# Performance work log

Measured on AMD Instinct MI355X. Metric: run time of the kernel, lower is better.

Reference implementation:

```python
import jax, jax.numpy as jnp
import numpy as np
import math

B, U, IN, H = 4096, 6, 256, 600
IKS, IVS, NIH = 64, 400, 1           # input attention key/value sizes, heads
CKS, CQS, NCH = 32, 32, 4            # comm attention key/query sizes, heads
CVS = H                              # comm value size forced to hidden_size
K = 4                                # top-k active units


@jax.custom_vjp
def blocked_grad(x, mask):
    return x

def _bg_fwd(x, mask):
    return x, mask

def _bg_bwd(mask, g):
    return (g * mask, jnp.zeros_like(mask))

blocked_grad.defvjp(_bg_fwd, _bg_bwd)


def _gll(x, w):
    # GroupLinearLayer: per-unit bmm, x (B,U,din) @ w (U,din,dout) -> (B,U,dout)
    return jnp.einsum('bud,udo->buo', x, w)


def setup_inputs() -> dict:
    key = jax.random.key(0)
    ks = jax.random.split(key, 16)
    r = lambda i, shape: (0.02 * jax.random.normal(ks[i], shape)).astype(jnp.float32)
    return dict(
        x=jax.random.normal(ks[0], (B, 1, IN), jnp.float32),
        hs=jax.random.normal(ks[1], (B, U, H), jnp.float32),
        Wk=r(2, (IN, NIH * IKS)), bk=jnp.zeros((NIH * IKS,), jnp.float32),
        Wv=r(3, (IN, NIH * IVS)), bv=jnp.zeros((NIH * IVS,), jnp.float32),
        Wq=r(4, (U, H, NIH * IKS)),
        x2h_w=r(5, (U, IVS, 3 * H)), h2h_w=r(6, (U, H, 3 * H)),
        Wq_=r(7, (U, H, NCH * CQS)), Wk_=r(8, (U, H, NCH * CKS)),
        Wv_=r(9, (U, H, NCH * CVS)), Wout=r(10, (U, NCH * CVS, CVS)),
    )


def reference(x, hs, Wk, bk, Wv, bv, Wq, x2h_w, h2h_w, Wq_, Wk_, Wv_, Wout):
    h_old = hs
    # append null input along dim 1 -> (B,2,IN)
    xcat = jnp.concatenate([x, jnp.zeros_like(x)], axis=1)
    # ---- input attention + top-k mask ----
    key_l = (xcat @ Wk + bk).reshape(B, 2, NIH, IKS).transpose(0, 2, 1, 3)   # (B,1,2,ks)
    val_l = (xcat @ Wv + bv).reshape(B, 2, NIH, IVS).mean(axis=2)             # (B,2,vs) mean over heads
    qry_l = _gll(hs, Wq).reshape(B, U, NIH, IKS).transpose(0, 2, 1, 3)        # (B,1,U,ks)
    scores = jnp.einsum('bhuk,bhnk->bhun', qry_l, key_l) / math.sqrt(IKS)
    scores = scores.mean(axis=1)                                               # (B,U,2)
    not_null = scores[:, :, 0]
    _, idx = jax.lax.top_k(not_null, K)                                        # (B,K)
    mask = jnp.zeros((B, U), jnp.float32).at[jnp.arange(B)[:, None], idx].set(1.0)
    probs = jax.nn.softmax(scores, axis=-1)                                    # dropout is identity (eval)
    inputs = jnp.einsum('bun,bnv->buv', probs, val_l) * mask[:, :, None]       # (B,U,vs)
    # ---- GroupGRU cell ----
    gx = _gll(inputs, x2h_w)
    gh = _gll(hs, h2h_w)
    i_r, i_i, i_n = jnp.split(gx, 3, axis=2)
    h_r, h_i, h_n = jnp.split(gh, 3, axis=2)
    rg = jax.nn.sigmoid(i_r + h_r)
    ig = jax.nn.sigmoid(i_i + h_i)
    ng = jnp.tanh(i_n + rg * h_n)
    hs = ng + ig * (hs - ng)
    # ---- communication attention (with blocked_grad) ----
    h_b = blocked_grad(hs, mask[:, :, None])
    q = _gll(h_b, Wq_).reshape(B, U, NCH, CQS).transpose(0, 2, 1, 3)   # (B,4,U,32)
    k = _gll(h_b, Wk_).reshape(B, U, NCH, CKS).transpose(0, 2, 1, 3)
    v = _gll(h_b, Wv_).reshape(B, U, NCH, CVS).transpose(0, 2, 1, 3)   # (B,4,U,600)
    att = jax.nn.softmax(jnp.einsum('bhuk,bhnk->bhun', q, k) / math.sqrt(CKS), axis=-1)
    att = att * mask[:, None, :, None]   # zero rows of inactive query units
    ctx = jnp.einsum('bhun,bhnv->bhuv', att, v).transpose(0, 2, 1, 3).reshape(B, U, NCH * CVS)
    ctx = _gll(ctx, Wout) + h_b
    m = mask[:, :, None]
    return m * ctx + (1.0 - m) * h_old
```

## Files before the change

### kernel.cpp

```cpp
#include <hip/hip_runtime.h>
#include <math.h>

typedef unsigned short u16;
typedef __attribute__((ext_vector_type(8))) short short8;
typedef __attribute__((ext_vector_type(4))) float f32x4;

constexpr int NB   = 4096;
constexpr int NU   = 6;
constexpr int NIN  = 256;
constexpr int NH   = 600;
constexpr int IKS  = 64;
constexpr int IVS  = 400;
constexpr int NCH  = 4;
constexpr int CVS  = 600;
constexpr int KTOP = 4;

constexpr int QKW  = 256;
constexpr int VW   = NCH * CVS;

constexpr int KG2   = 896;
constexpr int HOFS2 = 256;
constexpr int NGATE = 640;
constexpr int NROWS3= 3 * NGATE;
constexpr int KXP   = 448;
constexpr int KH    = 640;
constexpr int VN    = 2432;
constexpr int BC    = 2048;
constexpr int NCHUNK = NB / BC;

constexpr long OFF_KV   = 0;
constexpr long OFF_QRY  = OFF_KV   + (long)NB * IKS;
constexpr long OFF_C0   = OFF_QRY  + (long)NB * NU * IKS;
constexpr long OFF_C1   = OFF_C0   + (long)NB * NU;
constexpr long OFF_MASK = OFF_C1   + (long)NB * NU;
constexpr long OFF_QK   = OFF_MASK + (long)NB * NU;
constexpr long OFF_ATTW = OFF_QK   + (long)NB * NU * QKW;
constexpr long OFF_HNBF = OFF_ATTW + (long)NB * NCH * NU * NU;
constexpr long OFF_WQK  = OFF_HNBF + (long)NU * NB * KH / 2;
constexpr long OFF_WV   = OFF_WQK  + (long)NU * QKW * KH / 2;
constexpr long OFF_WOUT = OFF_WV   + (long)NU * VN * KH / 2;
constexpr long OFF_WVB  = OFF_WOUT + (long)NU * NGATE * VN / 2;
constexpr long OFF_TVEC = OFF_WVB  + (long)256 * KXP / 2;
constexpr long OFF_WGRU2= OFF_TVEC + (long)NU * NROWS3;
constexpr long OFF_AGRU2= OFF_WGRU2+ (long)NU * NROWS3 * KG2/2;
constexpr long OFF_WGRUX = OFF_AGRU2;
constexpr long OFF_VBUF  = OFF_WGRU2;

__device__ __forceinline__ u16 f2bf(float f) {
    unsigned int x = __float_as_uint(f);
    x += 0x7FFFu + ((x >> 16) & 1u);
    return (u16)(x >> 16);
}
__device__ __forceinline__ float bf2f(u16 u) {
    return __uint_as_float(((unsigned int)u) << 16);
}
__device__ __forceinline__ void gl_lds16(const u16* g, u16* l) {
    __builtin_amdgcn_global_load_lds(
        (const __attribute__((address_space(1))) void*)g,
        (__attribute__((address_space(3))) void*)l, 16, 0, 0);
}

#define WAITVM_(N) asm volatile("s_waitcnt vmcnt(" #N ")" ::: "memory")
#define WAITVM(N)  WAITVM_(N)
#define WAITLG()   asm volatile("s_waitcnt lgkmcnt(0)" ::: "memory")
#define SBAR()     do { __builtin_amdgcn_sched_barrier(0); \
                        __builtin_amdgcn_s_barrier();      \
                        __builtin_amdgcn_sched_barrier(0); } while (0)

__global__ __launch_bounds__(256)
void wtrans_kernel(const float* __restrict__ src, long s_u, int s_ld, int s_colofs,
                   int Ksrc, int Nsub,
                   u16* __restrict__ dst, long d_u, int d_ld, int d_nofs, int d_kofs,
                   int gdiv, int s_gcol, int d_gnofs)
{
    __shared__ float tile[32][33];
    int z = blockIdx.z;
    int u = z, g = 0;
    if (gdiv > 1) { u = z / gdiv; g = z % gdiv; }
    const int k0 = blockIdx.x * 32, n0 = blockIdx.y * 32;
    const int t  = threadIdx.x;
    const int scol = s_colofs + g * s_gcol;
    const int dnof = d_nofs + g * d_gnofs;
    const float* S = src + (long)u * s_u;
    u16* D = dst + (long)u * d_u;
    #pragma unroll
    for (int r = 0; r < 4; r++) {
        int kk = r * 8 + (t >> 5), nn = t & 31;
        float v = 0.f;
        if (k0 + kk < Ksrc && n0 + nn < Nsub)
            v = S[(long)(k0 + kk) * s_ld + scol + n0 + nn];
        tile[kk][nn] = v;
    }
    __syncthreads();
    #pragma unroll
    for (int r = 0; r < 4; r++) {
        int nn = r * 8 + (t >> 5), kk = t & 31;
        if (n0 + nn < Nsub)
            D[(long)(dnof + n0 + nn) * d_ld + d_kofs + k0 + kk] = f2bf(tile[kk][nn]);
    }
}

__global__ __launch_bounds__(256)
void wvbcast_kernel(const float* __restrict__ Wv, u16* __restrict__ wvb)
{
    int id = blockIdx.x * 256 + threadIdx.x;
    if (id >= 256 * KXP) return;
    int j = id / KXP, k = id % KXP;
    wvb[id] = (k < IVS) ? f2bf(Wv[(long)j * IVS + k]) : (u16)0;
}

__global__ __launch_bounds__(256)
void tvec_kernel(const u16* __restrict__ wgx, const float* __restrict__ bv,
                 float* __restrict__ tvec)
{
    const int wid  = threadIdx.x >> 6, lane = threadIdx.x & 63;
    const int r    = blockIdx.x * 4 + wid;
    if (r >= NU * NROWS3) return;
    const int k = lane * 8;
    float s = 0;
    if (k < IVS) {
        short8 v = *(const short8*)&wgx[(long)r * KXP + k];
        #pragma unroll
        for (int i = 0; i < 8; i++) s = fmaf(bf2f((u16)v[i]), bv[k + i], s);
    }
    #pragma unroll
    for (int off = 32; off > 0; off >>= 1) s += __shfl_down(s, off);
    if (lane == 0) tvec[r] = s;
}

__global__ __launch_bounds__(256)
void gemm_qry_kernel(const float* __restrict__ A,
                     const float* __restrict__ W,
                     const float* __restrict__ x,
                     const float* __restrict__ Wk,
                     const float* __restrict__ bk,
                     float* __restrict__ C,
                     float* __restrict__ kv)
{
    const int u  = blockIdx.z;
    const int m0 = blockIdx.x * 64;
    const int tid = threadIdx.x;
    const int tm = tid / 16, tn = tid % 16;
    constexpr int N = IKS;

    const bool isk0 = (u == NU);
    const int  K   = isk0 ? NIN : NH;
    const long lda = isk0 ? NIN : (long)NU * NH;
    const float* Au = isk0 ? x : (A + (long)u * NH);
    const float* Wu = isk0 ? Wk : (W + (long)u * NH * N);

    __shared__ __align__(16) float As[32][72];
    __shared__ __align__(16) float Ws[32][68];
    float acc[4][4] = {};

    for (int k0 = 0; k0 < K; k0 += 32) {
        #pragma unroll
        for (int s2 = 0; s2 < 2; s2++) {
            int s = tid * 2 + s2;
            int row = s >> 3, kc = s & 7;
            float4 v = {0,0,0,0};
            if (k0 + kc*4 < K)
                v = *(const float4*)&Au[(long)(m0 + row) * lda + k0 + kc * 4];
            As[kc*4+0][row] = v.x; As[kc*4+1][row] = v.y;
            As[kc*4+2][row] = v.z; As[kc*4+3][row] = v.w;
        }
        #pragma unroll
        for (int s2 = 0; s2 < 2; s2++) {
            int s = tid * 2 + s2;
            int kr = s >> 4, c4 = s & 15;
            float4 v = {0,0,0,0};
            if (k0 + kr < K)
                v = *(const float4*)&Wu[(long)(k0 + kr) * N + c4 * 4];
            *(float4*)&Ws[kr][c4*4] = v;
        }
        __syncthreads();
        #pragma unroll
        for (int kk = 0; kk < 32; kk++) {
            float4 a4 = *(const float4*)&As[kk][tm*4];
            float4 w4 = *(const float4*)&Ws[kk][tn*4];
            float av[4] = {a4.x,a4.y,a4.z,a4.w}, wv[4] = {w4.x,w4.y,w4.z,w4.w};
            #pragma unroll
            for (int i = 0; i < 4; i++)
                #pragma unroll
                for (int j = 0; j < 4; j++)
                    acc[i][j] = fmaf(av[i], wv[j], acc[i][j]);
        }
        __syncthreads();
    }
    #pragma unroll
    for (int i = 0; i < 4; i++) {
        int row = m0 + tm*4 + i;
        #pragma unroll
        for (int j = 0; j < 4; j++) {
            int c = tn*4 + j;
            if (isk0) kv[(long)row*N + c] = acc[i][j] + bk[c];
            else      C[(long)row*(NU*IKS) + (long)u*IKS + c] = acc[i][j];
        }
    }
}

__global__ __launch_bounds__(64)
void score_kernel(const float* __restrict__ qry, const float* __restrict__ kv,
                  const float* __restrict__ bk,
                  float* __restrict__ c0, float* __restrict__ c1,
                  float* __restrict__ maskf)
{
    const int b = blockIdx.x;
    const int t = threadIdx.x;
    __shared__ float s0s[NU], s1s[NU];

    float k0v = kv[(long)b*IKS + t];
    float bkv = bk[t];
    for (int u = 0; u < NU; u++) {
        float q  = qry[((long)b*NU + u)*IKS + t];
        float p0 = q * k0v, p1 = q * bkv;
        #pragma unroll
        for (int off = 32; off > 0; off >>= 1) {
            p0 += __shfl_down(p0, off);
            p1 += __shfl_down(p1, off);
        }
        if (t == 0) { s0s[u] = p0 * 0.125f; s1s[u] = p1 * 0.125f; }
    }
    __syncthreads();
    if (t < NU) {
        int u = t;
        float su = s0s[u];
        int rank = 0;
        #pragma unroll
        for (int j = 0; j < NU; j++) {
            float sj = s0s[j];
            if (sj > su || (sj == su && j < u)) rank++;
        }
        float m = (rank < KTOP) ? 1.0f : 0.0f;
        float a = s0s[u], bb = s1s[u];
        float mx = fmaxf(a, bb);
        float e0 = expf(a - mx), e1 = expf(bb - mx);
        float p0 = e0 / (e0 + e1);
        c0[(long)b*NU + u]    = m * p0;
        c1[(long)b*NU + u]    = m * (1.0f - p0);
        maskf[(long)b*NU + u] = m;
    }
}

__global__ __launch_bounds__(256)
void prep_gruA_kernel(const float* __restrict__ x, const float* __restrict__ hs,
                      const float* __restrict__ c0, u16* __restrict__ Ag)
{
    long id = (long)blockIdx.x * 256 + threadIdx.x;
    const long total = (long)NU * NB * (KG2 / 8);
    if (id >= total) return;
    int k8 = (int)(id % (KG2 / 8));
    int b  = (int)((id / (KG2 / 8)) % NB);
    int u  = (int)(id / ((long)(KG2 / 8) * NB));
    int k  = k8 * 8;
    u16 o[8];
    if (k < HOFS2) {
        float cv0 = c0[(long)b*NU + u];
        const float* xp = x + (long)b*NIN + k;
        #pragma unroll
        for (int i = 0; i < 8; i++) o[i] = f2bf(cv0 * xp[i]);
    } else if (k < HOFS2 + NH) {
        const float* hp = hs + ((long)b*NU + u)*NH + (k - HOFS2);
        #pragma unroll
        for (int i = 0; i < 8; i++) o[i] = f2bf(hp[i]);
    } else {
        #pragma unroll
        for (int i = 0; i < 8; i++) o[i] = 0;
    }
    *(short8*)&Ag[id * 8] = *(const short8*)o;
}

__global__ __launch_bounds__(256, 3)
void gru_mfma_kernel(const u16* __restrict__ Ag, const u16* __restrict__ Wg,
                     const float* __restrict__ tvec, const float* __restrict__ maskf,
                     const float* __restrict__ hs, u16* __restrict__ hnbf)
{
    const int u  = blockIdx.z;
    const int m0 = blockIdx.x * 128;
    const int n0 = blockIdx.y * 32;
    const int tid = threadIdx.x;
    const int wid = tid >> 6, lane = tid & 63;
    const int wm = wid >> 1, wn = wid & 1;
    const int lrow = lane & 15, lkq = lane >> 4;
    const int srow = lane >> 2;
    const int scs  = (((lane & 3) ^ ((lane >> 3) & 3)) * 8);
    const int cofs = ((lkq ^ ((lrow >> 1) & 3)) * 8);

    __shared__ __align__(16) u16 As[3][128 * 32];
    __shared__ __align__(16) u16 Bs[3][128 * 32];

    const u16* Au = Ag + (long)u * NB * KG2;
    const u16* Wu = Wg + (long)u * NROWS3 * KG2;

    f32x4 aR[4], aI[4], aNX[4], aNH[4];
    #pragma unroll
    for (int m = 0; m < 4; m++) {
        aR[m] = (f32x4){0,0,0,0}; aI[m] = (f32x4){0,0,0,0};
        aNX[m] = (f32x4){0,0,0,0}; aNH[m] = (f32x4){0,0,0,0};
    }

#define GSTAGE(BUF, T) do {                                                   \
        const long kk0 = (long)(T) * 32;                                      \
        _Pragma("unroll")                                                     \
        for (int i2 = 0; i2 < 2; i2++) {                                      \
            int R = wid*32 + i2*16;                                           \
            int row = R + srow;                                               \
            gl_lds16(Au + (long)(m0 + row)*KG2 + kk0 + scs,                   \
                     &As[BUF][R * 32]);                                       \
            int g = row >> 5; if (g > 2) g = 2;     \
            int rn = row & 31;                                                \
            gl_lds16(Wu + ((long)g*NGATE + n0 + rn)*KG2 + kk0 + scs,          \
                     &Bs[BUF][R * 32]);                                       \
        }                                                                     \
    } while (0)

#define GCOMPUTE(BUF, T) do {                                                 \
        __builtin_amdgcn_s_setprio(1);                                        \
        short8 af[4], bR, bI, bN;                                             \
        _Pragma("unroll")                                                     \
        for (int m = 0; m < 4; m++)                                           \
            af[m] = *(const short8*)&As[BUF][(wm*64 + m*16 + lrow)*32 + cofs];\
        {                                                                     \
            int nr = wn*16 + lrow;                                            \
            bR = *(const short8*)&Bs[BUF][(0*32 + nr)*32 + cofs];             \
            bI = *(const short8*)&Bs[BUF][(1*32 + nr)*32 + cofs];             \
            bN = *(const short8*)&Bs[BUF][(2*32 + nr)*32 + cofs];             \
        }                                                                     \
        _Pragma("unroll")                                                     \
        for (int m = 0; m < 4; m++) {                                         \
            aR[m] = __builtin_amdgcn_mfma_f32_16x16x32_bf16(af[m], bR, aR[m], 0, 0, 0); \
            aI[m] = __builtin_amdgcn_mfma_f32_16x16x32_bf16(af[m], bI, aI[m], 0, 0, 0); \
        }                                                                     \
        if ((T) < HOFS2/32) {                                                 \
            _Pragma("unroll")                                                 \
            for (int m = 0; m < 4; m++)                                       \
                aNX[m] = __builtin_amdgcn_mfma_f32_16x16x32_bf16(af[m], bN, aNX[m], 0, 0, 0); \
        } else {                                                              \
            _Pragma("unroll")                                                 \
            for (int m = 0; m < 4; m++)                                       \
                aNH[m] = __builtin_amdgcn_mfma_f32_16x16x32_bf16(af[m], bN, aNH[m], 0, 0, 0); \
        }                                                                     \
        __builtin_amdgcn_s_setprio(0);                                        \
    } while (0)

    constexpr int KSTEPS = KG2 / 32;
    GSTAGE(0, 0);
    int bc = 0, bn = 1;
    for (int t = 0; t < KSTEPS - 1; ++t) {
        GSTAGE(bn, t + 1);
        WAITVM(4); SBAR();
        GCOMPUTE(bc, t);
        bc = bn; bn = (bn == 2) ? 0 : bn + 1;
    }
    WAITVM(0); SBAR();
    GCOMPUTE(bc, KSTEPS - 1);
#undef GCOMPUTE
#undef GSTAGE

    const int col = n0 + wn*16 + lrow;
    float tR = 0, tI = 0, tN = 0;
    if (col < NH) {
        tR = tvec[(long)u*NROWS3 + col];
        tI = tvec[(long)u*NROWS3 + NGATE + col];
        tN = tvec[(long)u*NROWS3 + 2*NGATE + col];
    }
    #pragma unroll
    for (int m = 0; m < 4; m++) {
        #pragma unroll
        for (int r = 0; r < 4; r++) {
            int row = m0 + wm*64 + m*16 + lkq*4 + r;
            u16 ov = 0;
            if (col < NH) {
                float mk = maskf[(long)row*NU + u];
                float rg = 1.0f / (1.0f + expf(-(aR[m][r] + mk*tR)));
                float ig = 1.0f / (1.0f + expf(-(aI[m][r] + mk*tI)));
                float ng = tanhf(aNX[m][r] + mk*tN + rg * aNH[m][r]);
                float h  = hs[((long)row*NU + u)*NH + col];
                ov = f2bf(ng + ig * (h - ng));
            }
            hnbf[(long)u*NB*KH + (long)row*KH + col] = ov;
        }
    }
}

template<int EPI>
__global__ __launch_bounds__(256, 2)
void mfgemm_kernel(const u16* __restrict__ A, long sAu, int lda,
                   const u16* __restrict__ Bw, long sBu, int ldb,
                   float* __restrict__ Cf, u16* __restrict__ C16,
                   long sCu, int ldc, int ksteps,
                   const float* __restrict__ maskf,
                   const u16* __restrict__ hnbf,
                   const float* __restrict__ hs,
                   int bbase)
{
    const int u  = blockIdx.z;
    const int m0 = blockIdx.x * 128;
    const int n0 = blockIdx.y * 128;
    const int tid = threadIdx.x;
    const int wid = tid >> 6, lane = tid & 63;
    const int wm = wid >> 1, wn = wid & 1;
    const int lrow = lane & 15, lkq = lane >> 4;
    const int l8 = lane & 7, lr8 = lane >> 3;
    const int rsw = lrow & 7;

    __shared__ __align__(16) u16 As[2][128 * 64];
    __shared__ __align__(16) u16 Bs[2][128 * 64];

    const u16* Au = A + (long)u * sAu;
    const u16* Bu = Bw + (long)u * sBu;

    f32x4 acc[4][4];
    #pragma unroll
    for (int m = 0; m < 4; m++)
        #pragma unroll
        for (int n = 0; n < 4; n++) acc[m][n] = (f32x4){0,0,0,0};

#define MSTAGE(BUF, KS) do {                                                  \
        const long kk0 = (long)(KS) * 64;                                     \
        _Pragma("unroll")                                                     \
        for (int i2 = 0; i2 < 4; i2++) {                                      \
            int rw = i2*32 + wid*8 + lr8;                                     \
            int co = ((l8 ^ (rw & 7)) * 8);                                   \
            gl_lds16(Au + (long)(m0 + rw)*lda + kk0 + co,                     \
                     &As[BUF][(i2*32 + wid*8) * 64]);                         \
            gl_lds16(Bu + (long)(n0 + rw)*ldb + kk0 + co,                     \
                     &Bs[BUF][(i2*32 + wid*8) * 64]);                         \
        }                                                                     \
    } while (0)

#define MCOMPUTE(BUF) do {                                                    \
        __builtin_amdgcn_s_setprio(1);                                        \
        _Pragma("unroll")                                                     \
        for (int ks2 = 0; ks2 < 2; ks2++) {                                   \
            const int cofs = (((ks2*4 + lkq) ^ rsw) * 8);                     \
            short8 af[4], bfr[4];                                             \
            _Pragma("unroll")                                                 \
            for (int m = 0; m < 4; m++)                                       \
                af[m] = *(const short8*)&As[BUF][(wm*64 + m*16 + lrow)*64 + cofs]; \
            _Pragma("unroll")                                                 \
            for (int n = 0; n < 4; n++)                                       \
                bfr[n] = *(const short8*)&Bs[BUF][(wn*64 + n*16 + lrow)*64 + cofs]; \
            _Pragma("unroll")                                                 \
            for (int m = 0; m < 4; m++)                                       \
                _Pragma("unroll")                                             \
                for (int n = 0; n < 4; n++)                                   \
                    acc[m][n] = __builtin_amdgcn_mfma_f32_16x16x32_bf16(af[m], bfr[n], acc[m][n], 0, 0, 0); \
        }                                                                     \
        __builtin_amdgcn_s_setprio(0);                                        \
    } while (0)

#define MPH(BUF, T, W) do {                                                   \
        if ((T) + 1 < ksteps) MSTAGE((BUF)^1, (T)+1);                         \
        WAITVM(W); SBAR();                                                    \
        MCOMPUTE(BUF);                                                        \
        WAITLG(); SBAR();                                                     \
    } while (0)

    MSTAGE(0, 0);
    int t = 0;
    for (; t + 2 < ksteps; t += 2) { MPH(0, t, 8); MPH(1, t+1, 8); }
    if (t + 2 == ksteps) { MPH(0, t, 8); MPH(1, t+1, 0); }
    else                 { MPH(0, t, 0); }
#undef MPH
#undef MCOMPUTE
#undef MSTAGE

    #pragma unroll
    for (int m = 0; m < 4; m++) {
        #pragma unroll
        for (int r = 0; r < 4; r++) {
            int row = m0 + wm*64 + m*16 + lkq*4 + r;
            #pragma unroll
            for (int n = 0; n < 4; n++) {
                int col = n0 + wn*64 + n*16 + lrow;
                float v = acc[m][n][r];
                if (EPI == 0) {
                    Cf[(long)u*sCu + (long)row*ldc + col] = v;
                } else if (EPI == 2) {
                    C16[(long)u*sCu + (long)row*ldc + col] = f2bf(v);
                } else {
                    if (col < NH) {
                        int b = bbase + row;
                        long o = ((long)b*NU + u)*NH + col;
                        float mk = maskf[(long)b*NU + u];
                        float hv = bf2f(hnbf[(long)u*NB*KH + (long)b*KH + col]);
                        Cf[o] = (mk > 0.5f) ? (v + hv) : hs[o];
                    }
                }
            }
        }
    }
}

__global__ __launch_bounds__(256)
void attw_kernel(const float* __restrict__ qk, const float* __restrict__ maskf,
                 float* __restrict__ attw)
{
    const int b = blockIdx.x;
    const int t = threadIdx.x;
    __shared__ float qks[NU * QKW];
    __shared__ float lg[NCH][NU][NU];

    for (int i = t; i < NU * QKW / 4; i += 256)
        *(float4*)&qks[i * 4] = *(const float4*)&qk[(long)b * NU * QKW + i * 4];
    __syncthreads();

    if (t < NCH * NU * NU) {
        int h = t / 36, uq = (t % 36) / 6, un = t % 6;
        const float* qp = &qks[uq * QKW + h * 32];
        const float* kp = &qks[un * QKW + 128 + h * 32];
        float s = 0;
        #pragma unroll
        for (int i = 0; i < 32; i++) s = fmaf(qp[i], kp[i], s);
        lg[h][uq][un] = s * 0.17677669529663687f;
    }
    __syncthreads();
    if (t < NCH * NU) {
        int h = t / NU, uq = t % NU;
        float mx = -1e30f;
        #pragma unroll
        for (int n = 0; n < NU; n++) mx = fmaxf(mx, lg[h][uq][n]);
        float e[NU], se = 0;
        #pragma unroll
        for (int n = 0; n < NU; n++) { e[n] = expf(lg[h][uq][n] - mx); se += e[n]; }
        float m = maskf[(long)b*NU + uq];
        float inv = m / se;
        #pragma unroll
        for (int n = 0; n < NU; n++)
            attw[(((long)b*NCH + h)*NU + uq)*NU + n] = e[n] * inv;
    }
}

__global__ __launch_bounds__(256)
void ctx2_kernel(const float* __restrict__ attw, u16* vc, int bbase)
{
    __shared__ float att_s[32][NCH * NU * NU];
    const int c0 = blockIdx.x * 64;
    const int b0 = blockIdx.y * 32;
    const int tid = threadIdx.x;

    for (int i = tid; i < 32 * 144; i += 256) {
        int bl = i / 144, j = i % 144;
        att_s[bl][j] = attw[(long)(bbase + b0 + bl) * 144 + j];
    }
    __syncthreads();

    const int bl = tid >> 3;
    const int c  = c0 + (tid & 7) * 8;
    const long rowbase = (long)(b0 + bl) * NU;

    if (c >= VW) {
        short8 z = {0,0,0,0,0,0,0,0};
        #pragma unroll
        for (int u = 0; u < NU; u++)
            *(short8*)&vc[(rowbase + u) * VN + c] = z;
        return;
    }
    const int h = c / CVS;
    const float* aw = &att_s[bl][h * 36];

    float vf[NU][8];
    #pragma unroll
    for (int n = 0; n < NU; n++) {
        short8 vv = *(const short8*)&vc[(rowbase + n) * VN + c];
        #pragma unroll
        for (int i = 0; i < 8; i++) vf[n][i] = bf2f((u16)vv[i]);
    }
    #pragma unroll
    for (int u = 0; u < NU; u++) {
        float acc[8] = {};
        #pragma unroll
        for (int n = 0; n < NU; n++) {
            float a = aw[u * 6 + n];
            #pragma unroll
            for (int i = 0; i < 8; i++) acc[i] = fmaf(a, vf[n][i], acc[i]);
        }
        short8 o;
        #pragma unroll
        for (int i = 0; i < 8; i++) o[i] = (short)f2bf(acc[i]);
        *(short8*)&vc[(rowbase + u) * VN + c] = o;
    }
}

extern "C" void kernel_launch(void* const* d_in, const int* in_sizes, int n_in,
                              void* d_out, int out_size, void* d_ws, size_t ws_size,
                              hipStream_t stream)
{
    const float* x    = (const float*)d_in[0];
    const float* hs   = (const float*)d_in[1];
    const float* Wk   = (const float*)d_in[2];
    const float* bk   = (const float*)d_in[3];
    const float* Wv   = (const float*)d_in[4];
    const float* bv   = (const float*)d_in[5];
    const float* Wq   = (const float*)d_in[6];
    const float* x2h  = (const float*)d_in[7];
    const float* h2h  = (const float*)d_in[8];
    const float* Wq_  = (const float*)d_in[9];
    const float* Wk_  = (const float*)d_in[10];
    const float* Wv_  = (const float*)d_in[11];
    const float* Wout = (const float*)d_in[12];
    float* out = (float*)d_out;
    float* ws  = (float*)d_ws;

    float* kv    = ws + OFF_KV;
    float* qry   = ws + OFF_QRY;
    float* c0b   = ws + OFF_C0;
    float* c1b   = ws + OFF_C1;
    float* maskf = ws + OFF_MASK;
    float* qk    = ws + OFF_QK;
    float* attw  = ws + OFF_ATTW;
    u16*   hnbf  = (u16*)(ws + OFF_HNBF);
    u16*   wqk   = (u16*)(ws + OFF_WQK);
    u16*   wv    = (u16*)(ws + OFF_WV);
    u16*   wout  = (u16*)(ws + OFF_WOUT);
    u16*   wvb   = (u16*)(ws + OFF_WVB);
    float* tvec  = ws + OFF_TVEC;
    u16*   wgru2 = (u16*)(ws + OFF_WGRU2);
    u16*   agru2 = (u16*)(ws + OFF_AGRU2);
    u16*   wgx   = (u16*)(ws + OFF_WGRUX);
    u16*   vcbuf = (u16*)(ws + OFF_VBUF);

    wtrans_kernel<<<dim3(20, 4, NU), 256, 0, stream>>>(
        Wq_, (long)NH*128, 128, 0, NH, 128, wqk, (long)QKW*KH, KH, 0, 0, 1, 0, 0);
    wtrans_kernel<<<dim3(20, 4, NU), 256, 0, stream>>>(
        Wk_, (long)NH*128, 128, 0, NH, 128, wqk, (long)QKW*KH, KH, 128, 0, 1, 0, 0);
    wtrans_kernel<<<dim3(20, 75, NU), 256, 0, stream>>>(
        Wv_, (long)NH*VW, VW, 0, NH, VW, wv, (long)VN*KH, KH, 0, 0, 1, 0, 0);
    wtrans_kernel<<<dim3(76, 19, NU), 256, 0, stream>>>(
        Wout, (long)VW*NH, NH, 0, VW, NH, wout, (long)NGATE*VN, VN, 0, 0, 1, 0, 0);
    wtrans_kernel<<<dim3(KXP/32, 19, NU*3), 256, 0, stream>>>(
        x2h, (long)IVS*3*NH, 3*NH, 0, IVS, NH,
        wgx, (long)NROWS3*KXP, KXP, 0, 0, 3, NH, NGATE);
    wtrans_kernel<<<dim3(20, 19, NU*3), 256, 0, stream>>>(
        h2h, (long)NH*3*NH, 3*NH, 0, NH, NH,
        wgru2, (long)NROWS3*KG2, KG2, 0, HOFS2, 3, NH, NGATE);
    wvbcast_kernel<<<(256*KXP + 255)/256, 256, 0, stream>>>(Wv, wvb);
    mfgemm_kernel<2><<<dim3(NROWS3/128, 2, NU), 256, 0, stream>>>(
        wgx, (long)NROWS3*KXP, KXP, wvb, 0L, KXP,
        nullptr, wgru2, (long)NROWS3*KG2, KG2, KXP/64, nullptr, nullptr, nullptr, 0);
    tvec_kernel<<<(NU*NROWS3 + 3)/4, 256, 0, stream>>>(wgx, bv, tvec);

    gemm_qry_kernel<<<dim3(NB/64, 1, NU + 1), 256, 0, stream>>>(
        hs, Wq, x, Wk, bk, qry, kv);
    score_kernel<<<NB, 64, 0, stream>>>(qry, kv, bk, c0b, c1b, maskf);

    {
        long total = (long)NU * NB * (KG2/8);
        prep_gruA_kernel<<<(unsigned)((total + 255)/256), 256, 0, stream>>>(
            x, hs, c0b, agru2);
    }
    gru_mfma_kernel<<<dim3(NB/128, NGATE/32, NU), 256, 0, stream>>>(
        agru2, wgru2, tvec, maskf, hs, hnbf);

    mfgemm_kernel<0><<<dim3(NB/128, QKW/128, NU), 256, 0, stream>>>(
        hnbf, (long)NB*KH, KH, wqk, (long)QKW*KH, KH,
        qk, nullptr, (long)QKW, NU*QKW, KH/64, nullptr, nullptr, nullptr, 0);
    attw_kernel<<<NB, 256, 0, stream>>>(qk, maskf, attw);

    for (int ch = 0; ch < NCHUNK; ch++) {
        mfgemm_kernel<2><<<dim3(BC/128, VN/128, NU), 256, 0, stream>>>(
            hnbf + (long)ch*BC*KH, (long)NB*KH, KH, wv, (long)VN*KH, KH,
            nullptr, vcbuf, (long)VN, NU*VN, KH/64, nullptr, nullptr, nullptr, 0);
        ctx2_kernel<<<dim3(VN/64, BC/32), 256, 0, stream>>>(
            attw, vcbuf, ch*BC);
        mfgemm_kernel<1><<<dim3(BC/128, NGATE/128, NU), 256, 0, stream>>>(
            vcbuf, (long)VN, NU*VN, wout, (long)NGATE*VN, VN,
            out, nullptr, 0, 0, VN/64, maskf, hnbf, hs, ch*BC);
    }
}
```

Baseline: 682.5 us.

## Compact active (batch,unit) rows and run output GEMM only on them

The score kernel now atomically appends active batch indices per chunk and unit into a list. A new gathered-row GEMM computes the Wout projection only for those rows, and a separate kernel copies hs into the output for inactive rows. This is meant to skip about a third of the output GEMM work, since only 4 of 6 units are active. The cost is an extra copy kernel, atomics, and indirect row loads that ignore list order.

```diff
diff --git a/kernel.cpp b/kernel.cpp
--- a/kernel.cpp
+++ b/kernel.cpp
@@ -41,7 +41,9 @@
 constexpr long OFF_WOUT = OFF_WV   + (long)NU * VN * KH / 2;
 constexpr long OFF_WVB  = OFF_WOUT + (long)NU * NGATE * VN / 2;
 constexpr long OFF_TVEC = OFF_WVB  + (long)256 * KXP / 2;
-constexpr long OFF_WGRU2= OFF_TVEC + (long)NU * NROWS3;
+constexpr long OFF_CNT  = OFF_TVEC + (long)NU * NROWS3;
+constexpr long OFF_BLIST= OFF_CNT  + 16;
+constexpr long OFF_WGRU2= OFF_BLIST+ (long)NCHUNK * NU * BC;
 constexpr long OFF_AGRU2= OFF_WGRU2+ (long)NU * NROWS3 * KG2/2;
 constexpr long OFF_WGRUX = OFF_AGRU2;
 constexpr long OFF_VBUF  = OFF_WGRU2;
@@ -135,7 +137,8 @@
                      const float* __restrict__ Wk,
                      const float* __restrict__ bk,
                      float* __restrict__ C,
-                     float* __restrict__ kv)
+                     float* __restrict__ kv,
+                     int* __restrict__ cnt)
 {
     const int u  = blockIdx.z;
     const int m0 = blockIdx.x * 64;
@@ -144,6 +147,7 @@
     constexpr int N = IKS;
 
     const bool isk0 = (u == NU);
+    if (isk0 && blockIdx.x == 0 && tid < NCHUNK * NU) cnt[tid] = 0;
     const int  K   = isk0 ? NIN : NH;
     const long lda = isk0 ? NIN : (long)NU * NH;
     const float* Au = isk0 ? x : (A + (long)u * NH);
@@ -203,7 +207,8 @@
 void score_kernel(const float* __restrict__ qry, const float* __restrict__ kv,
                   const float* __restrict__ bk,
                   float* __restrict__ c0, float* __restrict__ c1,
-                  float* __restrict__ maskf)
+                  float* __restrict__ maskf,
+                  int* __restrict__ cnt, int* __restrict__ blist)
 {
     const int b = blockIdx.x;
     const int t = threadIdx.x;
@@ -239,6 +244,27 @@
         c0[(long)b*NU + u]    = m * p0;
         c1[(long)b*NU + u]    = m * (1.0f - p0);
         maskf[(long)b*NU + u] = m;
+        if (m > 0.5f) {
+            int ch  = b / BC;
+            int pos = atomicAdd(&cnt[ch*NU + u], 1);
+            blist[((long)ch*NU + u)*BC + pos] = b;
+        }
+    }
+}
+
+__global__ __launch_bounds__(256)
+void copy_unmasked_kernel(const float* __restrict__ hs,
+                          const float* __restrict__ maskf,
+                          float* __restrict__ out)
+{
+    long id = (long)blockIdx.x * 256 + threadIdx.x;
+    const long total = (long)NB * NU * (NH / 4);
+    if (id >= total) return;
+    int c4 = (int)(id % (NH / 4));
+    int bu = (int)(id / (NH / 4));
+    if (maskf[bu] < 0.5f) {
+        long o = (long)bu * NH + c4 * 4;
+        *(float4*)&out[o] = *(const float4*)&hs[o];
     }
 }
 
@@ -388,11 +414,7 @@
 void mfgemm_kernel(const u16* __restrict__ A, long sAu, int lda,
                    const u16* __restrict__ Bw, long sBu, int ldb,
                    float* __restrict__ Cf, u16* __restrict__ C16,
-                   long sCu, int ldc, int ksteps,
-                   const float* __restrict__ maskf,
-                   const u16* __restrict__ hnbf,
-                   const float* __restrict__ hs,
-                   int bbase)
+                   long sCu, int ldc, int ksteps)
 {
     const int u  = blockIdx.z;
     const int m0 = blockIdx.x * 128;
@@ -475,18 +497,114 @@
             for (int n = 0; n < 4; n++) {
                 int col = n0 + wn*64 + n*16 + lrow;
                 float v = acc[m][n][r];
-                if (EPI == 0) {
-                    Cf[(long)u*sCu + (long)row*ldc + col] = v;
-                } else if (EPI == 2) {
-                    C16[(long)u*sCu + (long)row*ldc + col] = f2bf(v);
-                } else {
-                    if (col < NH) {
-                        int b = bbase + row;
-                        long o = ((long)b*NU + u)*NH + col;
-                        float mk = maskf[(long)b*NU + u];
-                        float hv = bf2f(hnbf[(long)u*NB*KH + (long)b*KH + col]);
-                        Cf[o] = (mk > 0.5f) ? (v + hv) : hs[o];
-                    }
+                if (EPI == 0) Cf[(long)u*sCu + (long)row*ldc + col] = v;
+                else          C16[(long)u*sCu + (long)row*ldc + col] = f2bf(v);
+            }
+        }
+    }
+}
+
+__global__ __launch_bounds__(256, 2)
+void outc_kernel(const u16* __restrict__ vcbuf,
+                 const u16* __restrict__ wout,
+                 const int* __restrict__ cnt, const int* __restrict__ blist,
+                 const u16* __restrict__ hnbf, float* __restrict__ out,
+                 int ch)
+{
+    const int u  = blockIdx.z;
+    const int m0 = blockIdx.x * 128;
+    const int count = cnt[ch*NU + u];
+    if (m0 >= count) return;
+    const int* bl = blist + ((long)ch*NU + u)*BC;
+    const int bbase = ch * BC;
+    const int n0 = blockIdx.y * 128;
+    const int tid = threadIdx.x;
+    const int wid = tid >> 6, lane = tid & 63;
+    const int wm = wid >> 1, wn = wid & 1;
+    const int lrow = lane & 15, lkq = lane >> 4;
+    const int l8 = lane & 7, lr8 = lane >> 3;
+    const int rsw = lrow & 7;
+    constexpr int ksteps = VN / 64;
+
+    __shared__ __align__(16) u16 As[2][128 * 64];
+    __shared__ __align__(16) u16 Bs[2][128 * 64];
+
+    const u16* arp[4];
+    #pragma unroll
+    for (int i2 = 0; i2 < 4; i2++) {
+        int lr = m0 + i2*32 + wid*8 + lr8;
+        if (lr >= count) lr = count - 1;
+        int b = bl[lr];
+        arp[i2] = vcbuf + ((long)(b - bbase)*NU + u)*VN;
+    }
+    const u16* Bu = wout + (long)u * NGATE * VN;
+
+    f32x4 acc[4][4];
+    #pragma unroll
+    for (int m = 0; m < 4; m++)
+        #pragma unroll
+        for (int n = 0; n < 4; n++) acc[m][n] = (f32x4){0,0,0,0};
+
+#define OSTAGE(BUF, KS) do {                                                  \
+        const long kk0 = (long)(KS) * 64;                                     \
+        _Pragma("unroll")                                                     \
+        for (int i2 = 0; i2 < 4; i2++) {                                      \
+            int rw = i2*32 + wid*8 + lr8;                                     \
+            int co = ((l8 ^ (rw & 7)) * 8);                                   \
+            gl_lds16(arp[i2] + kk0 + co, &As[BUF][(i2*32 + wid*8) * 64]);     \
+            gl_lds16(Bu + (long)(n0 + rw)*VN + kk0 + co,                      \
+                     &Bs[BUF][(i2*32 + wid*8) * 64]);                         \
+        }                                                                     \
+    } while (0)
+
+#define OCOMPUTE(BUF) do {                                                    \
+        __builtin_amdgcn_s_setprio(1);                                        \
+        _Pragma("unroll")                                                     \
+        for (int ks2 = 0; ks2 < 2; ks2++) {                                   \
+            const int cofs = (((ks2*4 + lkq) ^ rsw) * 8);                     \
+            short8 af[4], bfr[4];                                             \
+            _Pragma("unroll")                                                 \
+            for (int m = 0; m < 4; m++)                                       \
+                af[m] = *(const short8*)&As[BUF][(wm*64 + m*16 + lrow)*64 + cofs]; \
+            _Pragma("unroll")                                                 \
+            for (int n = 0; n < 4; n++)                                       \
+                bfr[n] = *(const short8*)&Bs[BUF][(wn*64 + n*16 + lrow)*64 + cofs]; \
+            _Pragma("unroll")                                                 \
+            for (int m = 0; m < 4; m++)                                       \
+                _Pragma("unroll")                                             \
+                for (int n = 0; n < 4; n++)                                   \
+                    acc[m][n] = __builtin_amdgcn_mfma_f32_16x16x32_bf16(af[m], bfr[n], acc[m][n], 0, 0, 0); \
+        }                                                                     \
+        __builtin_amdgcn_s_setprio(0);                                        \
+    } while (0)
+
+    OSTAGE(0, 0);
+    int t = 0;
+    for (; t + 2 < ksteps; t += 2) {
+        if (t + 1 < ksteps) {}
+        OSTAGE(1, t + 1); WAITVM(8); SBAR(); OCOMPUTE(0); WAITLG(); SBAR();
+        if (t + 2 < ksteps) OSTAGE(0, t + 2);
+        WAITVM(8); SBAR(); OCOMPUTE(1); WAITLG(); SBAR();
+    }
+    OSTAGE(1, t + 1); WAITVM(8); SBAR(); OCOMPUTE(0); WAITLG(); SBAR();
+    WAITVM(0); SBAR(); OCOMPUTE(1); WAITLG(); SBAR();
+#undef OCOMPUTE
+#undef OSTAGE
+
+    #pragma unroll
+    for (int m = 0; m < 4; m++) {
+        #pragma unroll
+        for (int r = 0; r < 4; r++) {
+            int lr = m0 + wm*64 + m*16 + lkq*4 + r;
+            if (lr >= count) continue;
+            int b = bl[lr];
+            #pragma unroll
+            for (int n = 0; n < 4; n++) {
+                int col = n0 + wn*64 + n*16 + lrow;
+                if (col < NH) {
+                    long o = ((long)b*NU + u)*NH + col;
+                    float hv = bf2f(hnbf[(long)u*NB*KH + (long)b*KH + col]);
+                    out[o] = acc[m][n][r] + hv;
                 }
             }
         }
@@ -616,6 +734,8 @@
     u16*   wout  = (u16*)(ws + OFF_WOUT);
     u16*   wvb   = (u16*)(ws + OFF_WVB);
     float* tvec  = ws + OFF_TVEC;
+    int*   cnt   = (int*)(ws + OFF_CNT);
+    int*   blist = (int*)(ws + OFF_BLIST);
     u16*   wgru2 = (u16*)(ws + OFF_WGRU2);
     u16*   agru2 = (u16*)(ws + OFF_AGRU2);
     u16*   wgx   = (u16*)(ws + OFF_WGRUX);
@@ -638,12 +758,14 @@
     wvbcast_kernel<<<(256*KXP + 255)/256, 256, 0, stream>>>(Wv, wvb);
     mfgemm_kernel<2><<<dim3(NROWS3/128, 2, NU), 256, 0, stream>>>(
         wgx, (long)NROWS3*KXP, KXP, wvb, 0L, KXP,
-        nullptr, wgru2, (long)NROWS3*KG2, KG2, KXP/64, nullptr, nullptr, nullptr, 0);
+        nullptr, wgru2, (long)NROWS3*KG2, KG2, KXP/64);
     tvec_kernel<<<(NU*NROWS3 + 3)/4, 256, 0, stream>>>(wgx, bv, tvec);
 
     gemm_qry_kernel<<<dim3(NB/64, 1, NU + 1), 256, 0, stream>>>(
-        hs, Wq, x, Wk, bk, qry, kv);
-    score_kernel<<<NB, 64, 0, stream>>>(qry, kv, bk, c0b, c1b, maskf);
+        hs, Wq, x, Wk, bk, qry, kv, cnt);
+    score_kernel<<<NB, 64, 0, stream>>>(qry, kv, bk, c0b, c1b, maskf, cnt, blist);
+    copy_unmasked_kernel<<<(unsigned)(((long)NB*NU*(NH/4) + 255)/256), 256, 0, stream>>>(
+        hs, maskf, out);
 
     {
         long total = (long)NU * NB * (KG2/8);
@@ -655,17 +777,16 @@
 
     mfgemm_kernel<0><<<dim3(NB/128, QKW/128, NU), 256, 0, stream>>>(
         hnbf, (long)NB*KH, KH, wqk, (long)QKW*KH, KH,
-        qk, nullptr, (long)QKW, NU*QKW, KH/64, nullptr, nullptr, nullptr, 0);
+        qk, nullptr, (long)QKW, NU*QKW, KH/64);
     attw_kernel<<<NB, 256, 0, stream>>>(qk, maskf, attw);
 
     for (int ch = 0; ch < NCHUNK; ch++) {
         mfgemm_kernel<2><<<dim3(BC/128, VN/128, NU), 256, 0, stream>>>(
             hnbf + (long)ch*BC*KH, (long)NB*KH, KH, wv, (long)VN*KH, KH,
-            nullptr, vcbuf, (long)VN, NU*VN, KH/64, nullptr, nullptr, nullptr, 0);
+            nullptr, vcbuf, (long)VN, NU*VN, KH/64);
         ctx2_kernel<<<dim3(VN/64, BC/32), 256, 0, stream>>>(
             attw, vcbuf, ch*BC);
-        mfgemm_kernel<1><<<dim3(BC/128, NGATE/128, NU), 256, 0, stream>>>(
-            vcbuf, (long)VN, NU*VN, wout, (long)NGATE*VN, VN,
-            out, nullptr, 0, 0, VN/64, maskf, hnbf, hs, ch*BC);
-    }
-}
+        outc_kernel<<<dim3(BC/128, NGATE/128, NU), 256, 0, stream>>>(
+            vcbuf, wout, cnt, blist, hnbf, out, ch);
+    }
+}
```

After: 747.7 us. 9.6% more time.
